# Performance work log

Hardware: AMD Instinct MI355X
Metric: run time of the kernel (lower is better)

## Reference

```python
import jax, jax.numpy as jnp
import numpy as np

C = 256; M = 8; K = 4; L = 4; DFF = 1024; CV = C // M
SHAPES = [(100, 100), (50, 50), (25, 25), (13, 13)]
B = 16; LQ = 900


def setup_inputs() -> dict:
    key = jax.random.key(0)
    ks = iter(jax.random.split(key, 64))
    def n(shape, s=0.02):
        return jax.random.normal(next(ks), shape, jnp.float32) * s
    inp = {
        "query_objects": n((LQ, B, C), 1.0),
        "query_poses": n((LQ, B, C), 1.0),
        "ref_points": jax.random.uniform(next(ks), (LQ, B, 2), jnp.float32),
    }
    for i, (h, w) in enumerate(SHAPES):
        inp[f"feat{i}"] = n((B, h, w, C), 1.0)
        inp[f"pos{i}"] = n((B, h, w, C), 1.0)
    inp.update(dict(
        sa_in_w=n((C, 3 * C)), sa_in_b=jnp.zeros((3 * C,), jnp.float32),
        sa_out_w=n((C, C)), sa_out_b=jnp.zeros((C,), jnp.float32),
        n1_g=jnp.ones((C,), jnp.float32), n1_b=jnp.zeros((C,), jnp.float32),
        n2_g=jnp.ones((C,), jnp.float32), n2_b=jnp.zeros((C,), jnp.float32),
        n3_g=jnp.ones((C,), jnp.float32), n3_b=jnp.zeros((C,), jnp.float32),
        val_w=n((C, C)), val_b=jnp.zeros((C,), jnp.float32),
        off_w=n((C, M * L * K * 2)), off_b=n((M * L * K * 2,), 0.5),
        aw_w=n((C, M * L * K)), aw_b=jnp.zeros((M * L * K,), jnp.float32),
        dout_w=n((C, C)), dout_b=jnp.zeros((C,), jnp.float32),
        ffn_w1=n((C, DFF)), ffn_b1=jnp.zeros((DFF,), jnp.float32),
        ffn_w2=n((DFF, C)), ffn_b2=jnp.zeros((C,), jnp.float32),
    ))
    return inp


def layernorm(x, g, b, eps=1e-5):
    m = x.mean(-1, keepdims=True)
    v = ((x - m) ** 2).mean(-1, keepdims=True)
    return (x - m) * jax.lax.rsqrt(v + eps) * g + b


def mha(x_q, x_k, x_v, Win, bin_, Wout, bout):
    # torch nn.MultiheadAttention, seq-first (Lq, B, C), no masks, eval mode
    Lq, Bn, _ = x_q.shape
    q = (x_q @ Win[:, :C] + bin_[:C]).reshape(Lq, Bn, M, CV)
    k = (x_k @ Win[:, C:2 * C] + bin_[C:2 * C]).reshape(Lq, Bn, M, CV)
    v = (x_v @ Win[:, 2 * C:] + bin_[2 * C:]).reshape(Lq, Bn, M, CV)
    a = jax.nn.softmax(jnp.einsum('qbmd,kbmd->bmqk', q * (CV ** -0.5), k), axis=-1)
    o = jnp.einsum('bmqk,kbmd->qbmd', a, v).reshape(Lq, Bn, C)
    return o @ Wout + bout


def deform_attn(qd, ref, feats, val_w, val_b, off_w, off_b, aw_w, aw_b, dout_w, dout_b):
    # qd: (B, Lq, C) queries; ref: (B, Lq, 2) normalized [0,1] reference points (x, y)
    Bn, Lq, _ = qd.shape
    off = (qd @ off_w + off_b).reshape(Bn, Lq, M, L, K, 2)            # sampling offsets (pixels)
    aw = jax.nn.softmax((qd @ aw_w + aw_b).reshape(Bn, Lq, M, L * K), axis=-1)
    aw = aw.reshape(Bn, Lq, M, L, K)                                   # attention weights over L*K
    out = jnp.zeros((Bn, Lq, M, CV), qd.dtype)
    for l, feat in enumerate(feats):
        H, W = feat.shape[1], feat.shape[2]
        # shared value projection, split into heads: (B, M, HW, Cv)
        v = (feat.reshape(Bn, H * W, C) @ val_w + val_b).reshape(Bn, H * W, M, CV).transpose(0, 2, 1, 3)
        px = ref[:, :, None, None, 0] * W - 0.5 + off[:, :, :, l, :, 0]  # (B, Lq, M, K)
        py = ref[:, :, None, None, 1] * H - 0.5 + off[:, :, :, l, :, 1]
        x0 = jnp.floor(px); y0 = jnp.floor(py)
        samp = jnp.zeros((Bn, M, Lq, K, CV), qd.dtype)
        for dx in (0.0, 1.0):
            for dy in (0.0, 1.0):
                xi = x0 + dx; yi = y0 + dy
                wgt = (1.0 - jnp.abs(px - xi)) * (1.0 - jnp.abs(py - yi))
                valid = (xi >= 0) & (xi < W) & (yi >= 0) & (yi < H)      # zero padding outside
                idx = (jnp.clip(yi, 0, H - 1) * W + jnp.clip(xi, 0, W - 1)).astype(jnp.int32)
                idx_t = idx.transpose(0, 2, 1, 3).reshape(Bn, M, Lq * K)
                g = jnp.take_along_axis(v, idx_t[..., None], axis=2).reshape(Bn, M, Lq, K, CV)
                samp = samp + g * (wgt * valid).transpose(0, 2, 1, 3)[..., None]
        out = out + jnp.einsum('bqmk,bmqkc->bqmc', aw[:, :, :, l], samp)
    return out.reshape(Bn, Lq, C) @ dout_w + dout_b


def reference(query_objects, query_poses, ref_points, feat0, feat1, feat2, feat3,
              pos0, pos1, pos2, pos3, sa_in_w, sa_in_b, sa_out_w, sa_out_b,
              n1_g, n1_b, n2_g, n2_b, n3_g, n3_b, val_w, val_b, off_w, off_b,
              aw_w, aw_b, dout_w, dout_b, ffn_w1, ffn_b1, ffn_w2, ffn_b2):
    # post-norm decoder layer, eval mode (dropout = identity)
    q = query_objects + query_poses
    x = query_objects + mha(q, q, query_objects, sa_in_w, sa_in_b, sa_out_w, sa_out_b)
    x = layernorm(x, n1_g, n1_b)
    feats = [feat0 + pos0, feat1 + pos1, feat2 + pos2, feat3 + pos3]
    qd = x.transpose(1, 0, 2)              # (B, Lq, C)
    ref = ref_points.transpose(1, 0, 2)    # (B, Lq, 2)
    d = deform_attn(qd, ref, feats, val_w, val_b, off_w, off_b, aw_w, aw_b, dout_w, dout_b)
    x = x + d.transpose(1, 0, 2)
    x = layernorm(x, n2_g, n2_b)
    x = x + (jax.nn.relu(x @ ffn_w1 + ffn_b1) @ ffn_w2 + ffn_b2)
    x = layernorm(x, n3_g, n3_b)
    return x
```

## Files before the change

### kernel.cpp

```cpp
#include <hip/hip_runtime.h>
#include <hip/hip_bf16.h>
#include <cstdint>

#define LQ 900
#define BB 16
#define CC 256
#define MM 8
#define CV 32
#define NROWS (LQ * BB)

typedef __attribute__((ext_vector_type(8))) short short8;
typedef __attribute__((ext_vector_type(4))) float f32x4;

__device__ __forceinline__ short f2bf(float f) {
    union { float f; unsigned u; } x; x.f = f;
    const unsigned r = x.u + 0x7fff + ((x.u >> 16) & 1);
    return (short)(r >> 16);
}
__device__ __forceinline__ float bf2f(ushort u) {
    union { unsigned u; float f; } c; c.u = ((unsigned)u) << 16; return c.f;
}

__device__ __constant__ int d_HW[4]    = {100, 50, 25, 13};
__device__ __constant__ int d_baseR[4] = {0, 160000, 200000, 210000};

__global__ __launch_bounds__(256) void conv_w_T(
    const float* __restrict__ W, ushort* __restrict__ Wt, int K, int N)
{
    __shared__ float tl[32][33];
    const int t = threadIdx.x;
    const int tx = t & 31, ty = t >> 5;
    const int n0 = blockIdx.x * 32, k0 = blockIdx.y * 32;
    #pragma unroll
    for (int p = 0; p < 4; ++p)
        tl[ty + 8 * p][tx] = W[(size_t)(k0 + ty + 8 * p) * N + n0 + tx];
    __syncthreads();
    #pragma unroll
    for (int p = 0; p < 4; ++p)
        Wt[(size_t)(n0 + ty + 8 * p) * K + k0 + tx] = (ushort)f2bf(tl[tx][ty + 8 * p]);
}

__global__ void concat_bias(const float* __restrict__ a, const float* __restrict__ b,
                            float* __restrict__ o)
{
    const int t = blockIdx.x * 256 + threadIdx.x;
    if (t < 384) o[t] = (t < 256) ? a[t] : b[t - 256];
}

template<bool A_BF16, bool ADD_A2, bool RELU, bool RESID, bool OUT_BF16>
__global__ __launch_bounds__(256) void gemm_bf16(
    const void* __restrict__ Ap, const float* __restrict__ A2, int lda,
    const ushort* __restrict__ Bt, const float* __restrict__ bias,
    const float* __restrict__ resid, void* __restrict__ Cp, int ldc,
    int Mr, int Kd)
{
    __shared__ ushort lds[16384];
    ushort* As = lds;
    ushort* Bs = lds + 8192;

    const int t = threadIdx.x;
    const int lane = t & 63;
    const int w = t >> 6;
    const int wr = w >> 1, wc = w & 1;
    const int lr = lane & 15, lk = lane >> 4;
    const int row0 = blockIdx.y * 128;
    const int col0 = blockIdx.x * 128;

    f32x4 acc[4][4] = {};

    const int srow = t >> 4;
    const int skq  = (t & 15) * 4;
    const int sg   = (t & 15) >> 1;
    const int srem = (t & 1) * 8;

    const float*  Af = (const float*)Ap;
    const ushort* Ah = (const ushort*)Ap;

    short4 sa_[8], sb_[8];
    float4 fa_[8], f2_[8];

    const int nk = Kd >> 6;

    auto issue = [&](int kk0) {
        #pragma unroll
        for (int p = 0; p < 8; ++p) {
            const int gr = min(row0 + p * 16 + srow, Mr - 1);
            if constexpr (A_BF16) {
                sa_[p] = *reinterpret_cast<const short4*>(Ah + (size_t)gr * lda + kk0 + skq);
            } else {
                fa_[p] = *reinterpret_cast<const float4*>(Af + (size_t)gr * lda + kk0 + skq);
                if constexpr (ADD_A2)
                    f2_[p] = *reinterpret_cast<const float4*>(A2 + (size_t)gr * lda + kk0 + skq);
            }
            sb_[p] = *reinterpret_cast<const short4*>(Bt + (size_t)(col0 + p * 16 + srow) * Kd + kk0 + skq);
        }
    };

    issue(0);

    for (int kt = 0; kt < nk; ++kt) {
        #pragma unroll
        for (int p = 0; p < 8; ++p) {
            const int r = p * 16 + srow;
            short4 a4;
            if constexpr (A_BF16) {
                a4 = sa_[p];
            } else {
                float4 av = fa_[p];
                if constexpr (ADD_A2) {
                    av.x += f2_[p].x; av.y += f2_[p].y; av.z += f2_[p].z; av.w += f2_[p].w;
                }
                a4.x = f2bf(av.x); a4.y = f2bf(av.y); a4.z = f2bf(av.z); a4.w = f2bf(av.w);
            }
            const int byteA = r * 128 + ((sg ^ (r & 7)) << 4) + srem;
            *reinterpret_cast<short4*>((char*)As + byteA) = a4;
            *reinterpret_cast<short4*>((char*)Bs + byteA) = sb_[p];
        }
        __syncthreads();

        if (kt + 1 < nk) issue((kt + 1) * 64);

        #pragma unroll
        for (int kk = 0; kk < 2; ++kk) {
            short8 af[4], bfr[4];
            #pragma unroll
            for (int i = 0; i < 4; ++i) {
                const int r = wr * 64 + i * 16 + lr;
                const int byte = r * 128 + (((kk * 4 + lk) ^ (r & 7)) << 4);
                af[i] = *reinterpret_cast<const short8*>((char*)As + byte);
            }
            #pragma unroll
            for (int j = 0; j < 4; ++j) {
                const int r = wc * 64 + j * 16 + lr;
                const int byte = r * 128 + (((kk * 4 + lk) ^ (r & 7)) << 4);
                bfr[j] = *reinterpret_cast<const short8*>((char*)Bs + byte);
            }
            #pragma unroll
            for (int i = 0; i < 4; ++i)
                #pragma unroll
                for (int j = 0; j < 4; ++j)
                    acc[i][j] = __builtin_amdgcn_mfma_f32_16x16x32_bf16(af[i], bfr[j], acc[i][j], 0, 0, 0);
        }
        __syncthreads();
    }

    if constexpr (OUT_BF16) {
        ushort* Cb = (ushort*)Cp;
        #pragma unroll
        for (int j = 0; j < 4; ++j) {
            const int lcol = wc * 64 + j * 16 + lr;
            const float bcol = bias[col0 + lcol];
            #pragma unroll
            for (int i = 0; i < 4; ++i) {
                const int lrbase = wr * 64 + i * 16 + lk * 4;
                #pragma unroll
                for (int reg = 0; reg < 4; ++reg) {
                    float v = acc[i][j][reg] + bcol;
                    if (RELU) v = fmaxf(v, 0.f);
                    lds[(lrbase + reg) * 128 + lcol] = (ushort)f2bf(v);
                }
            }
        }
        __syncthreads();
        const int erow = t >> 1, ehalf = t & 1;
        if (row0 + erow < Mr) {
            ushort* dst = Cb + (size_t)(row0 + erow) * ldc + col0 + ehalf * 64;
            const ushort* src = lds + erow * 128 + ehalf * 64;
            #pragma unroll
            for (int q = 0; q < 8; ++q)
                *reinterpret_cast<short8*>(dst + q * 8) =
                    *reinterpret_cast<const short8*>(src + q * 8);
        }
    } else {
        float* Cf = (float*)Cp;
        #pragma unroll
        for (int j = 0; j < 4; ++j) {
            const int col = col0 + wc * 64 + j * 16 + lr;
            const float bcol = bias[col];
            #pragma unroll
            for (int i = 0; i < 4; ++i) {
                const int rbase = row0 + wr * 64 + i * 16 + lk * 4;
                #pragma unroll
                for (int reg = 0; reg < 4; ++reg) {
                    const int r = rbase + reg;
                    if (r < Mr) {
                        float v = acc[i][j][reg] + bcol;
                        if (RESID) v += resid[(size_t)r * ldc + col];
                        if (RELU)  v = fmaxf(v, 0.f);
                        Cf[(size_t)r * ldc + col] = v;
                    }
                }
            }
        }
    }
}

__global__ __launch_bounds__(256) void attn_mfma(
    const ushort* __restrict__ QKbf, const ushort* __restrict__ Vbf,
    ushort* __restrict__ attnO)
{
    __shared__ ushort K_lds[64][40];
    __shared__ ushort Vt[32][72];
    __shared__ ushort P_lds[4][16][72];

    const int t = threadIdx.x;
    const int w = t >> 6, lane = t & 63;
    const int q0 = blockIdx.x * 64;
    const int m = blockIdx.y & 7, b = blockIdx.y >> 3;

    const int lr = lane & 15;
    const int lk = lane >> 4;

    const int qrow = min(q0 + w * 16 + lr, LQ - 1);
    const short8 qf = *reinterpret_cast<const short8*>(
        QKbf + ((size_t)qrow * BB + b) * 512 + m * 32 + lk * 8);

    f32x4 oacc[2] = {f32x4{0.f,0.f,0.f,0.f}, f32x4{0.f,0.f,0.f,0.f}};
    float mrun[4] = {-1e30f, -1e30f, -1e30f, -1e30f};
    float lrun[4] = {0.f, 0.f, 0.f, 0.f};

    const float scale = 0.17677669529663687f;
    const int sr = t >> 2;
    const int sd = (t & 3) * 8;

    for (int k0 = 0; k0 < LQ; k0 += 64) {
        {
            const int kr = min(k0 + sr, LQ - 1);
            *reinterpret_cast<short8*>(&K_lds[sr][sd]) =
                *reinterpret_cast<const short8*>(QKbf + ((size_t)kr * BB + b) * 512 + 256 + m * 32 + sd);
            const short8 v8 = *reinterpret_cast<const short8*>(
                Vbf + ((size_t)kr * BB + b) * 256 + m * 32 + sd);
            #pragma unroll
            for (int j = 0; j < 8; ++j) Vt[sd + j][sr] = (ushort)v8[j];
        }
        __syncthreads();

        f32x4 sa[4];
        #pragma unroll
        for (int n = 0; n < 4; ++n) {
            const short8 kf = *reinterpret_cast<const short8*>(&K_lds[n * 16 + lr][lk * 8]);
            sa[n] = __builtin_amdgcn_mfma_f32_16x16x32_bf16(qf, kf, f32x4{0.f,0.f,0.f,0.f}, 0, 0, 0);
        }
        #pragma unroll
        for (int n = 0; n < 4; ++n)
            #pragma unroll
            for (int r = 0; r < 4; ++r)
                sa[n][r] *= scale;
        if (k0 + 64 > LQ) {
            #pragma unroll
            for (int n = 0; n < 4; ++n)
                if (k0 + n * 16 + lr >= LQ) {
                    #pragma unroll
                    for (int r = 0; r < 4; ++r) sa[n][r] = -1e30f;
                }
        }

        #pragma unroll
        for (int r = 0; r < 4; ++r) {
            float mx = fmaxf(fmaxf(sa[0][r], sa[1][r]), fmaxf(sa[2][r], sa[3][r]));
            #pragma unroll
            for (int o = 8; o; o >>= 1) mx = fmaxf(mx, __shfl_xor(mx, o));
            const float mnew = fmaxf(mrun[r], mx);
            const float corr = __expf(mrun[r] - mnew);
            mrun[r] = mnew;
            float psum = 0.f;
            #pragma unroll
            for (int n = 0; n < 4; ++n) {
                const float p = __expf(sa[n][r] - mnew);
                psum += p;
                P_lds[w][lk * 4 + r][n * 16 + lr] = (ushort)f2bf(p);
            }
            #pragma unroll
            for (int o = 8; o; o >>= 1) psum += __shfl_xor(psum, o);
            lrun[r] = lrun[r] * corr + psum;
            oacc[0][r] *= corr;
            oacc[1][r] *= corr;
        }

        #pragma unroll
        for (int kk = 0; kk < 2; ++kk) {
            const short8 pf = *reinterpret_cast<const short8*>(&P_lds[w][lr][kk * 32 + lk * 8]);
            #pragma unroll
            for (int dt = 0; dt < 2; ++dt) {
                const short8 vf = *reinterpret_cast<const short8*>(&Vt[dt * 16 + lr][kk * 32 + lk * 8]);
                oacc[dt] = __builtin_amdgcn_mfma_f32_16x16x32_bf16(pf, vf, oacc[dt], 0, 0, 0);
            }
        }
        __syncthreads();
    }

    #pragma unroll
    for (int r = 0; r < 4; ++r) {
        const int row = q0 + w * 16 + lk * 4 + r;
        if (row < LQ) {
            const float inv = 1.f / lrun[r];
            ushort* op = attnO + ((size_t)row * BB + b) * 256 + m * 32;
            op[lr]      = (ushort)f2bf(oacc[0][r] * inv);
            op[16 + lr] = (ushort)f2bf(oacc[1][r] * inv);
        }
    }
}

__global__ __launch_bounds__(256) void ln_kernel(
    const float* __restrict__ X, const float* __restrict__ g,
    const float* __restrict__ bta, float* __restrict__ Y, int nrows)
{
    const int r = blockIdx.x * 4 + (threadIdx.x >> 6);
    if (r >= nrows) return;
    const int lane = threadIdx.x & 63;
    const float4 v = *reinterpret_cast<const float4*>(X + (size_t)r * 256 + lane * 4);
    float s  = v.x + v.y + v.z + v.w;
    float sq = v.x * v.x + v.y * v.y + v.z * v.z + v.w * v.w;
    #pragma unroll
    for (int o = 32; o; o >>= 1) { s += __shfl_xor(s, o); sq += __shfl_xor(sq, o); }
    const float mean = s * (1.f / 256.f);
    const float var  = sq * (1.f / 256.f) - mean * mean;
    const float rs   = rsqrtf(var + 1e-5f);
    const float4 gv = *reinterpret_cast<const float4*>(g + lane * 4);
    const float4 bv = *reinterpret_cast<const float4*>(bta + lane * 4);
    float4 o4;
    o4.x = (v.x - mean) * rs * gv.x + bv.x;
    o4.y = (v.y - mean) * rs * gv.y + bv.y;
    o4.z = (v.z - mean) * rs * gv.z + bv.z;
    o4.w = (v.w - mean) * rs * gv.w + bv.w;
    *reinterpret_cast<float4*>(Y + (size_t)r * 256 + lane * 4) = o4;
}

__global__ __launch_bounds__(256) void samp_prep(
    const float* __restrict__ ref, const float* __restrict__ obf,
    int4* __restrict__ prepI, float4* __restrict__ prepW)
{
    const int gid = blockIdx.x * 256 + threadIdx.x;
    const int k = gid & 3, l = (gid >> 2) & 3, m = (gid >> 4) & 7, row = gid >> 7;
    const int b = row & 15;

    const float logit = obf[(size_t)row * 384 + 256 + m * 16 + l * 4 + k];
    float mx = logit;
    #pragma unroll
    for (int o = 1; o < 16; o <<= 1) mx = fmaxf(mx, __shfl_xor(mx, o));
    const float e = __expf(logit - mx);
    float se = e;
    #pragma unroll
    for (int o = 1; o < 16; o <<= 1) se += __shfl_xor(se, o);
    const float aw = e / se;

    const int   Hl = d_HW[l];
    const float Hf = (float)Hl;
    const int   gbase = d_baseR[l] + b * Hl * Hl;
    const float rx = ref[row * 2 + 0], ry = ref[row * 2 + 1];
    const float ox = obf[(size_t)row * 384 + m * 32 + l * 8 + k * 2 + 0];
    const float oy = obf[(size_t)row * 384 + m * 32 + l * 8 + k * 2 + 1];
    const float px = rx * Hf - 0.5f + ox;
    const float py = ry * Hf - 0.5f + oy;
    const float x0 = floorf(px), y0 = floorf(py);

    int4 I; float4 W;
    #pragma unroll
    for (int c = 0; c < 4; ++c) {
        const float xi = x0 + (float)(c & 1);
        const float yi = y0 + (float)(c >> 1);
        const float wv = (1.f - fabsf(px - xi)) * (1.f - fabsf(py - yi));
        const bool valid = (xi >= 0.f) && (xi < Hf) && (yi >= 0.f) && (yi < Hf);
        const int ix = min(max((int)xi, 0), Hl - 1);
        const int iy = min(max((int)yi, 0), Hl - 1);
        const int idx = gbase + iy * Hl + ix;
        const float wgt = valid ? aw * wv : 0.f;
        if (c == 0) { I.x = idx; W.x = wgt; }
        else if (c == 1) { I.y = idx; W.y = wgt; }
        else if (c == 2) { I.z = idx; W.z = wgt; }
        else { I.w = idx; W.w = wgt; }
    }
    prepI[gid] = I;
    prepW[gid] = W;
}

__global__ __launch_bounds__(256) void samp_gather(
    const ushort* __restrict__ Vval, const int4* __restrict__ prepI,
    const float4* __restrict__ prepW, float* __restrict__ samp)
{
    const int wid  = blockIdx.x * 4 + (threadIdx.x >> 6);
    const int lane = threadIdx.x & 63;
    const int q  = wid % LQ;
    const int bm = wid / LQ;
    const int m  = bm & 7, b = bm >> 3;
    const int row = q * BB + b;
    const int sid = lane >> 4, d2 = lane & 15;

    const uint* V2 = (const uint*)Vval;
    const int pbase = (row * 8 + m) * 16;
    const int coff  = m * 16 + d2;

    float a0 = 0.f, a1 = 0.f;
    #pragma unroll
    for (int g = 0; g < 4; ++g) {
        const int4   I = prepI[pbase + g * 4 + sid];
        const float4 W = prepW[pbase + g * 4 + sid];
        uint v;
        v = V2[(size_t)I.x * 128 + coff];
        a0 += W.x * bf2f((ushort)v); a1 += W.x * bf2f((ushort)(v >> 16));
        v = V2[(size_t)I.y * 128 + coff];
        a0 += W.y * bf2f((ushort)v); a1 += W.y * bf2f((ushort)(v >> 16));
        v = V2[(size_t)I.z * 128 + coff];
        a0 += W.z * bf2f((ushort)v); a1 += W.z * bf2f((ushort)(v >> 16));
        v = V2[(size_t)I.w * 128 + coff];
        a0 += W.w * bf2f((ushort)v); a1 += W.w * bf2f((ushort)(v >> 16));
    }
    a0 += __shfl_xor(a0, 16); a0 += __shfl_xor(a0, 32);
    a1 += __shfl_xor(a1, 16); a1 += __shfl_xor(a1, 32);
    if (lane < 16) {
        float2 o2; o2.x = a0; o2.y = a1;
        *reinterpret_cast<float2*>(samp + (size_t)row * 256 + m * 32 + d2 * 2) = o2;
    }
}

extern "C" void kernel_launch(void* const* d_in, const int* in_sizes, int n_in,
                              void* d_out, int out_size, void* d_ws, size_t ws_size,
                              hipStream_t stream)
{
    const float* qo   = (const float*)d_in[0];
    const float* qpz  = (const float*)d_in[1];
    const float* refp = (const float*)d_in[2];
    const float* feat[4] = {(const float*)d_in[3], (const float*)d_in[5],
                            (const float*)d_in[7], (const float*)d_in[9]};
    const float* pos[4]  = {(const float*)d_in[4], (const float*)d_in[6],
                            (const float*)d_in[8], (const float*)d_in[10]};
    const float* sa_in_w  = (const float*)d_in[11];
    const float* sa_in_b  = (const float*)d_in[12];
    const float* sa_out_w = (const float*)d_in[13];
    const float* sa_out_b = (const float*)d_in[14];
    const float* n1_g = (const float*)d_in[15];
    const float* n1_b = (const float*)d_in[16];
    const float* n2_g = (const float*)d_in[17];
    const float* n2_b = (const float*)d_in[18];
    const float* n3_g = (const float*)d_in[19];
    const float* n3_b = (const float*)d_in[20];
    const float* val_w  = (const float*)d_in[21];
    const float* val_b  = (const float*)d_in[22];
    const float* off_w  = (const float*)d_in[23];
    const float* off_b  = (const float*)d_in[24];
    const float* aw_w   = (const float*)d_in[25];
    const float* aw_b   = (const float*)d_in[26];
    const float* dout_w = (const float*)d_in[27];
    const float* dout_b = (const float*)d_in[28];
    const float* ffn_w1 = (const float*)d_in[29];
    const float* ffn_b1 = (const float*)d_in[30];
    const float* ffn_w2 = (const float*)d_in[31];
    const float* ffn_b2 = (const float*)d_in[32];

    char* ws = (char*)d_ws;
    ushort* QKbf   = (ushort*)(ws + 0);
    ushort* Vbf    = (ushort*)(ws + 14745600);
    ushort* attnO  = (ushort*)(ws + 22118400);
    ushort* Vval   = (ushort*)(ws + 29491200);
    ushort* WsaInT = (ushort*)(ws + 138395648);
    ushort* WsaOutT= (ushort*)(ws + 138788864);
    ushort* WvalT  = (ushort*)(ws + 138919936);
    ushort* WdoutT = (ushort*)(ws + 139051008);
    ushort* Wffn1T = (ushort*)(ws + 139182080);
    ushort* Wffn2T = (ushort*)(ws + 139706368);
    ushort* WoffAwT= (ushort*)(ws + 140230656);
    float*  obias  = (float*)(ws + 140427264);
    float* x1   = (float*)(ws + 140429312);
    float* dres = x1;
    float* xln1 = (float*)(ws + 155174912);
    float* obf  = (float*)(ws + 169920512);
    float* x3   = obf;
    float* samp = (float*)(ws + 192038912);
    float* xln2 = (float*)(ws + 206784512);
    ushort* h   = (ushort*)(ws + 221530112);
    int4*  prepI = (int4*)(ws + 251021312);
    float4* prepW = (float4*)(ws + 280512512);

    const dim3 blk(256);
    const int GM = (NROWS + 127) / 128;

    conv_w_T<<<dim3(24, 8), blk, 0, stream>>>(sa_in_w, WsaInT, 256, 768);
    conv_w_T<<<dim3(8, 8), blk, 0, stream>>>(sa_out_w, WsaOutT, 256, 256);
    conv_w_T<<<dim3(8, 8), blk, 0, stream>>>(val_w, WvalT, 256, 256);
    conv_w_T<<<dim3(8, 8), blk, 0, stream>>>(dout_w, WdoutT, 256, 256);
    conv_w_T<<<dim3(32, 8), blk, 0, stream>>>(ffn_w1, Wffn1T, 256, 1024);
    conv_w_T<<<dim3(8, 32), blk, 0, stream>>>(ffn_w2, Wffn2T, 1024, 256);
    conv_w_T<<<dim3(8, 8), blk, 0, stream>>>(off_w, WoffAwT, 256, 256);
    conv_w_T<<<dim3(4, 8), blk, 0, stream>>>(aw_w, WoffAwT + 256 * 256, 256, 128);
    concat_bias<<<dim3(2), blk, 0, stream>>>(off_b, aw_b, obias);

    gemm_bf16<false, true, false, false, true><<<dim3(4, GM), blk, 0, stream>>>(
        qo, qpz, 256, WsaInT, sa_in_b, nullptr, QKbf, 512, NROWS, 256);
    gemm_bf16<false, false, false, false, true><<<dim3(2, GM), blk, 0, stream>>>(
        qo, nullptr, 256, WsaInT + 512 * 256, sa_in_b + 512, nullptr, Vbf, 256, NROWS, 256);
    attn_mfma<<<dim3(15, 128), blk, 0, stream>>>(QKbf, Vbf, attnO);
    gemm_bf16<true, false, false, true, false><<<dim3(2, GM), blk, 0, stream>>>(
        attnO, nullptr, 256, WsaOutT, sa_out_b, qo, x1, 256, NROWS, 256);
    ln_kernel<<<dim3(3600), blk, 0, stream>>>(x1, n1_g, n1_b, xln1, NROWS);
    gemm_bf16<false, false, false, false, false><<<dim3(3, GM), blk, 0, stream>>>(
        xln1, nullptr, 256, WoffAwT, obias, nullptr, obf, 384, NROWS, 256);
    samp_prep<<<dim3(7200), blk, 0, stream>>>(refp, obf, prepI, prepW);
    gemm_bf16<false, true, false, false, true><<<dim3(2, 1250), blk, 0, stream>>>(
        feat[0], pos[0], 256, WvalT, val_b, nullptr, Vval, 256, 160000, 256);
    gemm_bf16<false, true, false, false, true><<<dim3(2, 313), blk, 0, stream>>>(
        feat[1], pos[1], 256, WvalT, val_b, nullptr, Vval + (size_t)160000 * 256, 256, 40000, 256);
    gemm_bf16<false, true, false, false, true><<<dim3(2, 79), blk, 0, stream>>>(
        feat[2], pos[2], 256, WvalT, val_b, nullptr, Vval + (size_t)200000 * 256, 256, 10000, 256);
    gemm_bf16<false, true, false, false, true><<<dim3(2, 22), blk, 0, stream>>>(
        feat[3], pos[3], 256, WvalT, val_b, nullptr, Vval + (size_t)210000 * 256, 256, 2704, 256);
    samp_gather<<<dim3(28800), blk, 0, stream>>>(Vval, prepI, prepW, samp);
    gemm_bf16<false, false, false, true, false><<<dim3(2, GM), blk, 0, stream>>>(
        samp, nullptr, 256, WdoutT, dout_b, xln1, dres, 256, NROWS, 256);
    ln_kernel<<<dim3(3600), blk, 0, stream>>>(dres, n2_g, n2_b, xln2, NROWS);
    gemm_bf16<false, false, true, false, true><<<dim3(8, GM), blk, 0, stream>>>(
        xln2, nullptr, 256, Wffn1T, ffn_b1, nullptr, h, 1024, NROWS, 256);
    gemm_bf16<true, false, false, true, false><<<dim3(2, GM), blk, 0, stream>>>(
        h, nullptr, 1024, Wffn2T, ffn_b2, xln2, x3, 256, NROWS, 1024);
    ln_kernel<<<dim3(3600), blk, 0, stream>>>(x3, n3_g, n3_b, (float*)d_out, NROWS);
}
```

Before: 601.2 us.

## Merge per-level value GEMMs, pad epilogue LDS, widen gather loads

The four value-projection GEMM launches are folded into one grouped kernel that picks the feature level from blockIdx.y. This removes launch overhead and the tail effects of the small levels. The bf16 epilogue staging buffer gets a padded row stride (136 instead of 128) to reduce LDS bank conflicts, which costs a slightly larger shared allocation. The sampling gather now loads 4 bf16 per lane (uint2) with 8 lanes per sample group and shuffle-reduces over 8/16/32, halving the number of gather loop iterations.

After: 606.6 us. No clear change (+0.9%).

```diff
diff --git a/kernel.cpp b/kernel.cpp
--- a/kernel.cpp
+++ b/kernel.cpp
@@ -47,14 +47,17 @@
     if (t < 384) o[t] = (t < 256) ? a[t] : b[t - 256];
 }
 
+#define EPS 136
+#define LDSN 17408
+
 template<bool A_BF16, bool ADD_A2, bool RELU, bool RESID, bool OUT_BF16>
-__global__ __launch_bounds__(256) void gemm_bf16(
+__device__ __forceinline__ void gemm_core(
+    ushort* lds,
     const void* __restrict__ Ap, const float* __restrict__ A2, int lda,
     const ushort* __restrict__ Bt, const float* __restrict__ bias,
     const float* __restrict__ resid, void* __restrict__ Cp, int ldc,
-    int Mr, int Kd)
-{
-    __shared__ ushort lds[16384];
+    int Mr, int Kd, int row0, int col0)
+{
     ushort* As = lds;
     ushort* Bs = lds + 8192;
 
@@ -63,8 +66,6 @@
     const int w = t >> 6;
     const int wr = w >> 1, wc = w & 1;
     const int lr = lane & 15, lk = lane >> 4;
-    const int row0 = blockIdx.y * 128;
-    const int col0 = blockIdx.x * 128;
 
     f32x4 acc[4][4] = {};
 
@@ -157,7 +158,7 @@
                 for (int reg = 0; reg < 4; ++reg) {
                     float v = acc[i][j][reg] + bcol;
                     if (RELU) v = fmaxf(v, 0.f);
-                    lds[(lrbase + reg) * 128 + lcol] = (ushort)f2bf(v);
+                    lds[(lrbase + reg) * EPS + lcol] = (ushort)f2bf(v);
                 }
             }
         }
@@ -165,7 +166,7 @@
         const int erow = t >> 1, ehalf = t & 1;
         if (row0 + erow < Mr) {
             ushort* dst = Cb + (size_t)(row0 + erow) * ldc + col0 + ehalf * 64;
-            const ushort* src = lds + erow * 128 + ehalf * 64;
+            const ushort* src = lds + erow * EPS + ehalf * 64;
             #pragma unroll
             for (int q = 0; q < 8; ++q)
                 *reinterpret_cast<short8*>(dst + q * 8) =
@@ -193,6 +194,40 @@
             }
         }
     }
+}
+
+template<bool A_BF16, bool ADD_A2, bool RELU, bool RESID, bool OUT_BF16>
+__global__ __launch_bounds__(256) void gemm_bf16(
+    const void* __restrict__ Ap, const float* __restrict__ A2, int lda,
+    const ushort* __restrict__ Bt, const float* __restrict__ bias,
+    const float* __restrict__ resid, void* __restrict__ Cp, int ldc,
+    int Mr, int Kd)
+{
+    __shared__ ushort lds[LDSN];
+    gemm_core<A_BF16, ADD_A2, RELU, RESID, OUT_BF16>(
+        lds, Ap, A2, lda, Bt, bias, resid, Cp, ldc, Mr, Kd,
+        blockIdx.y * 128, blockIdx.x * 128);
+}
+
+__global__ __launch_bounds__(256) void val_gemm(
+    const float* __restrict__ f0, const float* __restrict__ p0,
+    const float* __restrict__ f1, const float* __restrict__ p1,
+    const float* __restrict__ f2, const float* __restrict__ p2,
+    const float* __restrict__ f3, const float* __restrict__ p3,
+    const ushort* __restrict__ Bt, const float* __restrict__ bias,
+    ushort* __restrict__ Vval)
+{
+    __shared__ ushort lds[LDSN];
+    int by = blockIdx.y;
+    const float *Af, *A2;
+    int Mr, obase;
+    if (by < 1250)      { Af = f0; A2 = p0; Mr = 160000; obase = 0;      }
+    else if (by < 1563) { Af = f1; A2 = p1; Mr = 40000;  obase = 160000; by -= 1250; }
+    else if (by < 1642) { Af = f2; A2 = p2; Mr = 10000;  obase = 200000; by -= 1563; }
+    else                { Af = f3; A2 = p3; Mr = 2704;   obase = 210000; by -= 1642; }
+    gemm_core<false, true, false, false, true>(
+        lds, Af, A2, 256, Bt, bias, nullptr,
+        Vval + (size_t)obase * 256, 256, Mr, 256, by * 128, blockIdx.x * 128);
 }
 
 __global__ __launch_bounds__(256) void attn_mfma(
@@ -384,32 +419,40 @@
     const int bm = wid / LQ;
     const int m  = bm & 7, b = bm >> 3;
     const int row = q * BB + b;
-    const int sid = lane >> 4, d2 = lane & 15;
-
-    const uint* V2 = (const uint*)Vval;
+    const int sid = lane >> 3, dg = lane & 7;
+
+    const uint2* V4 = (const uint2*)Vval;
     const int pbase = (row * 8 + m) * 16;
-    const int coff  = m * 16 + d2;
-
-    float a0 = 0.f, a1 = 0.f;
-    #pragma unroll
-    for (int g = 0; g < 4; ++g) {
-        const int4   I = prepI[pbase + g * 4 + sid];
-        const float4 W = prepW[pbase + g * 4 + sid];
-        uint v;
-        v = V2[(size_t)I.x * 128 + coff];
-        a0 += W.x * bf2f((ushort)v); a1 += W.x * bf2f((ushort)(v >> 16));
-        v = V2[(size_t)I.y * 128 + coff];
-        a0 += W.y * bf2f((ushort)v); a1 += W.y * bf2f((ushort)(v >> 16));
-        v = V2[(size_t)I.z * 128 + coff];
-        a0 += W.z * bf2f((ushort)v); a1 += W.z * bf2f((ushort)(v >> 16));
-        v = V2[(size_t)I.w * 128 + coff];
-        a0 += W.w * bf2f((ushort)v); a1 += W.w * bf2f((ushort)(v >> 16));
-    }
-    a0 += __shfl_xor(a0, 16); a0 += __shfl_xor(a0, 32);
-    a1 += __shfl_xor(a1, 16); a1 += __shfl_xor(a1, 32);
-    if (lane < 16) {
-        float2 o2; o2.x = a0; o2.y = a1;
-        *reinterpret_cast<float2*>(samp + (size_t)row * 256 + m * 32 + d2 * 2) = o2;
+    const int coff  = m * 8 + dg;
+
+    float a0 = 0.f, a1 = 0.f, a2 = 0.f, a3 = 0.f;
+    #pragma unroll
+    for (int g = 0; g < 2; ++g) {
+        const int s = g * 8 + sid;
+        const int4   I = prepI[pbase + s];
+        const float4 W = prepW[pbase + s];
+        uint2 v;
+        v = V4[(size_t)I.x * 64 + coff];
+        a0 += W.x * bf2f((ushort)v.x); a1 += W.x * bf2f((ushort)(v.x >> 16));
+        a2 += W.x * bf2f((ushort)v.y); a3 += W.x * bf2f((ushort)(v.y >> 16));
+        v = V4[(size_t)I.y * 64 + coff];
+        a0 += W.y * bf2f((ushort)v.x); a1 += W.y * bf2f((ushort)(v.x >> 16));
+        a2 += W.y * bf2f((ushort)v.y); a3 += W.y * bf2f((ushort)(v.y >> 16));
+        v = V4[(size_t)I.z * 64 + coff];
+        a0 += W.z * bf2f((ushort)v.x); a1 += W.z * bf2f((ushort)(v.x >> 16));
+        a2 += W.z * bf2f((ushort)v.y); a3 += W.z * bf2f((ushort)(v.y >> 16));
+        v = V4[(size_t)I.w * 64 + coff];
+        a0 += W.w * bf2f((ushort)v.x); a1 += W.w * bf2f((ushort)(v.x >> 16));
+        a2 += W.w * bf2f((ushort)v.y); a3 += W.w * bf2f((ushort)(v.y >> 16));
+    }
+    #pragma unroll
+    for (int o = 8; o <= 32; o <<= 1) {
+        a0 += __shfl_xor(a0, o); a1 += __shfl_xor(a1, o);
+        a2 += __shfl_xor(a2, o); a3 += __shfl_xor(a3, o);
+    }
+    if (sid == 0) {
+        float4 o4; o4.x = a0; o4.y = a1; o4.z = a2; o4.w = a3;
+        *reinterpret_cast<float4*>(samp + (size_t)row * 256 + m * 32 + dg * 4) = o4;
     }
 }
 
@@ -495,14 +538,9 @@
     gemm_bf16<false, false, false, false, false><<<dim3(3, GM), blk, 0, stream>>>(
         xln1, nullptr, 256, WoffAwT, obias, nullptr, obf, 384, NROWS, 256);
     samp_prep<<<dim3(7200), blk, 0, stream>>>(refp, obf, prepI, prepW);
-    gemm_bf16<false, true, false, false, true><<<dim3(2, 1250), blk, 0, stream>>>(
-        feat[0], pos[0], 256, WvalT, val_b, nullptr, Vval, 256, 160000, 256);
-    gemm_bf16<false, true, false, false, true><<<dim3(2, 313), blk, 0, stream>>>(
-        feat[1], pos[1], 256, WvalT, val_b, nullptr, Vval + (size_t)160000 * 256, 256, 40000, 256);
-    gemm_bf16<false, true, false, false, true><<<dim3(2, 79), blk, 0, stream>>>(
-        feat[2], pos[2], 256, WvalT, val_b, nullptr, Vval + (size_t)200000 * 256, 256, 10000, 256);
-    gemm_bf16<false, true, false, false, true><<<dim3(2, 22), blk, 0, stream>>>(
-        feat[3], pos[3], 256, WvalT, val_b, nullptr, Vval + (size_t)210000 * 256, 256, 2704, 256);
+    val_gemm<<<dim3(2, 1664), blk, 0, stream>>>(
+        feat[0], pos[0], feat[1], pos[1], feat[2], pos[2], feat[3], pos[3],
+        WvalT, val_b, Vval);
     samp_gather<<<dim3(28800), blk, 0, stream>>>(Vval, prepI, prepW, samp);
     gemm_bf16<false, false, false, true, false><<<dim3(2, GM), blk, 0, stream>>>(
         samp, nullptr, 256, WdoutT, dout_b, xln1, dres, 256, NROWS, 256);
```
